# Performance work log

Hardware: AMD Instinct MI355X
Metric: run time of the kernel (lower is better)

Reference implementation:

```python
import jax, jax.numpy as jnp
import numpy as np

K, D, B = 2048, 50257, 256
N_CLASS = 2

def setup_inputs() -> dict:
    key = jax.random.key(0)
    k1, k2, k3 = jax.random.split(key, 3)
    # strictly positive (probability-like) entries so log() is finite
    queue_anchor = jax.random.uniform(k1, (K, D), dtype=jnp.float32, minval=1e-3, maxval=1.0)
    query = jax.random.uniform(k2, (B, D), dtype=jnp.float32, minval=1e-3, maxval=1.0)
    queue_label = jax.random.randint(k3, (K,), 0, N_CLASS, dtype=jnp.int64)
    return {"query": query, "queue_anchor": queue_anchor, "queue_label": queue_label}

def reference(query, queue_anchor, queue_label):
    # torch code: mean_d( a[:,None,:] * (log a[:,None,:] - log q) ).T  -> [B, K]
    # algebraically identical, avoiding the (K,B,D) intermediate:
    #   kl[b,k] = mean_d(a_k * log a_k) - (1/D) * sum_d a_k[d] * log q_b[d]
    d = queue_anchor.shape[1]
    self_term = jnp.mean(queue_anchor * jnp.log(queue_anchor), axis=1)        # [K]
    cross_term = jnp.einsum('kd,bd->kb', queue_anchor, jnp.log(query)) / d    # [K, B]
    kl_distance = (self_term[:, None] - cross_term).T                          # [B, K]
    # knn == 1 path: nearest anchor's label per query
    return queue_label[jnp.argmin(kl_distance, axis=1)]                        # [B]
```

## Files before the change

kernel.cpp:

```cpp
#include <hip/hip_runtime.h>


constexpr int K    = 2048;
constexpr int D    = 50257;
constexpr int B    = 256;
constexpr int DSPL = 25344;
constexpr int NC   = 8;
constexpr float MARGIN = 4.0f;

typedef __attribute__((ext_vector_type(8))) short bf16x8;
typedef __attribute__((ext_vector_type(4))) float f32x4;
typedef __attribute__((ext_vector_type(8))) unsigned short u16x8;

__device__ inline unsigned short f2bf_rne(float f) {
    union { float f; unsigned u; } v; v.f = f;
    unsigned r = v.u + 0x7FFFu + ((v.u >> 16) & 1u);
    return (unsigned short)(r >> 16);
}

__global__ __launch_bounds__(256)
void lq_kernel(const float* __restrict__ q, unsigned short* __restrict__ lq,
               int aoff, int DL, int nch)
{
    const int stride = gridDim.x * blockDim.x;
    const int total  = nch * B * 4;
    for (int c = blockIdx.x * blockDim.x + threadIdx.x; c < total; c += stride) {
        const int sub = c & 3;
        const int b   = (c >> 2) & 255;
        const int ch  = c >> 10;
        const int d0  = ch * 32 + sub * 8;
        u16x8 w;
#pragma unroll
        for (int j = 0; j < 8; ++j) {
            const int d = d0 + j;
            const float v = (d < DL) ? q[(size_t)b * D + aoff + d] : 1.f;
            w[j] = f2bf_rne(__logf(v));
        }
        *reinterpret_cast<u16x8*>(&lq[((size_t)ch * B + b) * 32 + sub * 8]) = w;
    }
}

__global__ __launch_bounds__(512)
void gemm_kernel(const float* __restrict__ anchor,
                 const unsigned short* __restrict__ lq,
                 float* __restrict__ part,
                 float* __restrict__ selfp,
                 int dc, int DL, int DCAP, int aoff, int zoff)
{
    const int nb8 = gridDim.x >> 3;
    const int g   = (blockIdx.x & 7) * nb8 + (blockIdx.x >> 3);
    const int z   = g >> 6;
    const int kt  = g & 63;
    const int k0  = kt * 32;

    const int t    = threadIdx.x;
    const int wid  = t >> 6;
    const int lane = t & 63;
    const int lr   = lane & 15;
    const int lg   = lane >> 4;

    const int zd0 = z * dc;
    const int zd1 = min(zd0 + dc, DCAP);
    const int wd  = ((dc / 8) + 31) & ~31;
    const int d0  = zd0 + wid * wd;
    const int d1  = min(d0 + wd, zd1);

    const size_t KDm4 = (size_t)K * D - 4;

    f32x4 acc0[16], acc1[16];
#pragma unroll
    for (int j = 0; j < 16; ++j)
#pragma unroll
        for (int i = 0; i < 4; ++i) { acc0[j][i] = 0.f; acc1[j][i] = 0.f; }

    float sacc0 = 0.f, sacc1 = 0.f;

    if (d0 < d1) {
        const int ar0 = k0 + lr;
        const int ar1 = ar0 + 16;
        const size_t gA0 = (size_t)ar0 * D + aoff + d0 + lg * 8;
        const size_t gA1 = (size_t)ar1 * D + aoff + d0 + lg * 8;
        const int ph0 = (int)(gA0 & 3);
        const int ph1 = (int)(gA1 & 3);
        size_t iA0 = gA0 - ph0;
        size_t iA1 = gA1 - ph1;

        const unsigned short* qp =
            lq + ((size_t)(d0 >> 5) * (B * 32) + (size_t)lr * 32 + lg * 8);

        auto ld4 = [&](size_t fi) -> float4 {
            if (fi > KDm4) fi = KDm4;
            return *reinterpret_cast<const float4*>(anchor + fi);
        };

        for (int dd = d0; dd < d1; dd += 32) {
            const int dbase = dd + lg * 8;
            bf16x8 af0, af1;
            {
                const float4 v0 = ld4(iA0), v1 = ld4(iA0 + 4), v2 = ld4(iA0 + 8);
                float wf[12] = {v0.x, v0.y, v0.z, v0.w, v1.x, v1.y, v1.z, v1.w,
                                v2.x, v2.y, v2.z, v2.w};
                float s9[9];
#pragma unroll
                for (int j = 0; j < 9; ++j) s9[j] = (ph0 & 2) ? wf[j + 2] : wf[j];
#pragma unroll
                for (int j = 0; j < 8; ++j) {
                    float a = (ph0 & 1) ? s9[j + 1] : s9[j];
                    a = (dbase + j < DL) ? a : 0.f;
                    if (a > 0.f) sacc0 = fmaf(a, __logf(a), sacc0);
                    af0[j] = (short)f2bf_rne(a);
                }
                iA0 += 32;
            }
            {
                const float4 v0 = ld4(iA1), v1 = ld4(iA1 + 4), v2 = ld4(iA1 + 8);
                float wf[12] = {v0.x, v0.y, v0.z, v0.w, v1.x, v1.y, v1.z, v1.w,
                                v2.x, v2.y, v2.z, v2.w};
                float s9[9];
#pragma unroll
                for (int j = 0; j < 9; ++j) s9[j] = (ph1 & 2) ? wf[j + 2] : wf[j];
#pragma unroll
                for (int j = 0; j < 8; ++j) {
                    float a = (ph1 & 1) ? s9[j + 1] : s9[j];
                    a = (dbase + j < DL) ? a : 0.f;
                    if (a > 0.f) sacc1 = fmaf(a, __logf(a), sacc1);
                    af1[j] = (short)f2bf_rne(a);
                }
                iA1 += 32;
            }
            {
                bf16x8 qf[8];
#pragma unroll
                for (int j = 0; j < 8; ++j)
                    qf[j] = *reinterpret_cast<const bf16x8*>(qp + j * 512);
#pragma unroll
                for (int j = 0; j < 8; ++j) {
                    acc0[j] = __builtin_amdgcn_mfma_f32_16x16x32_bf16(af0, qf[j], acc0[j], 0, 0, 0);
                    acc1[j] = __builtin_amdgcn_mfma_f32_16x16x32_bf16(af1, qf[j], acc1[j], 0, 0, 0);
                }
#pragma unroll
                for (int j = 0; j < 8; ++j)
                    qf[j] = *reinterpret_cast<const bf16x8*>(qp + (8 + j) * 512);
#pragma unroll
                for (int j = 0; j < 8; ++j) {
                    acc0[8 + j] = __builtin_amdgcn_mfma_f32_16x16x32_bf16(af0, qf[j], acc0[8 + j], 0, 0, 0);
                    acc1[8 + j] = __builtin_amdgcn_mfma_f32_16x16x32_bf16(af1, qf[j], acc1[8 + j], 0, 0, 0);
                }
            }
            qp += (size_t)B * 32;
        }
    }

    sacc0 += __shfl_xor(sacc0, 16); sacc0 += __shfl_xor(sacc0, 32);
    sacc1 += __shfl_xor(sacc1, 16); sacc1 += __shfl_xor(sacc1, 32);

    __shared__ __align__(16) float red[4][256 * 36];
    __shared__ float sred[8][32];

    if (lane < 16) { sred[wid][lr] = sacc0; sred[wid][16 + lr] = sacc1; }

    const int rbase = wid & 3;
    if (wid < 4) {
#pragma unroll
        for (int bt = 0; bt < 16; ++bt) {
            float* p0 = &red[rbase][(bt * 16 + lr) * 36 + lg * 4];
            *reinterpret_cast<f32x4*>(p0)      = acc0[bt];
            *reinterpret_cast<f32x4*>(p0 + 16) = acc1[bt];
        }
    }
    __syncthreads();
    if (wid >= 4) {
#pragma unroll
        for (int bt = 0; bt < 16; ++bt) {
            float* p0 = &red[rbase][(bt * 16 + lr) * 36 + lg * 4];
            f32x4 v0 = *reinterpret_cast<f32x4*>(p0);
            f32x4 v1 = *reinterpret_cast<f32x4*>(p0 + 16);
#pragma unroll
            for (int i = 0; i < 4; ++i) { v0[i] += acc0[bt][i]; v1[i] += acc1[bt][i]; }
            *reinterpret_cast<f32x4*>(p0)      = v0;
            *reinterpret_cast<f32x4*>(p0 + 16) = v1;
        }
    }
    __syncthreads();
    for (int i = t; i < 256 * 36; i += 512) {
        red[0][i] += red[2][i];
        red[1][i] += red[3][i];
    }
    __syncthreads();
    for (int i = t; i < 256 * 36; i += 512) red[0][i] += red[1][i];
    if (t < 32) {
        float s = 0.f;
#pragma unroll
        for (int w8 = 0; w8 < 8; ++w8) s += sred[w8][t];
        selfp[(size_t)(zoff + z) * K + k0 + t] = s;
    }
    __syncthreads();
    for (int i = t; i < 2048; i += 512) {
        const int b  = i >> 3;
        const int kq = i & 7;
        const f32x4 v = *reinterpret_cast<f32x4*>(&red[0][b * 36 + kq * 4]);
        *reinterpret_cast<f32x4*>(&part[((size_t)z * B + b) * K + k0 + kq * 4]) = v;
    }
}

__global__ __launch_bounds__(256)
void reduce_kernel(const float* __restrict__ part, float* __restrict__ crossA, int pch)
{
    const int i = blockIdx.x * 256 + threadIdx.x;
    const f32x4* p4 = reinterpret_cast<const f32x4*>(part);
    f32x4 s = p4[i];
    for (int z = 1; z < pch; ++z) {
        const f32x4 v = p4[(size_t)z * (B * K / 4) + i];
#pragma unroll
        for (int j = 0; j < 4; ++j) s[j] += v[j];
    }
    reinterpret_cast<f32x4*>(crossA)[i] = s;
}

__global__ __launch_bounds__(256)
void selfsum_kernel(const float* __restrict__ selfp, float* __restrict__ selftot, int rows)
{
    const int k = blockIdx.x * 256 + threadIdx.x;
    float s = 0.f;
    for (int z = 0; z < rows; ++z) s += selfp[(size_t)z * K + k];
    selftot[k] = s;
}

__global__ __launch_bounds__(256)
void topk_kernel(const float* __restrict__ crossA, const float* __restrict__ part,
                 const float* __restrict__ selftot,
                 int* __restrict__ cand, int* __restrict__ need, int pch)
{
    const int b = blockIdx.x, t = threadIdx.x;
    float v[8];
#pragma unroll
    for (int i = 0; i < 8; ++i) {
        const int k = i * 256 + t;
        float cv = crossA[(size_t)b * K + k];
        for (int z = 0; z < pch; ++z) cv += part[((size_t)z * B + b) * K + k];
        v[i] = selftot[k] - cv;
    }
    __shared__ float sv[256];
    __shared__ int   si[256];
    __shared__ float topv[2];
    for (int r = 0; r < NC; ++r) {
        float bv = 3.4e38f; int bk = K;
#pragma unroll
        for (int i = 0; i < 8; ++i) {
            const int k = i * 256 + t;
            if (v[i] < bv) { bv = v[i]; bk = k; }
        }
        sv[t] = bv; si[t] = bk;
        __syncthreads();
        for (int off = 128; off > 0; off >>= 1) {
            if (t < off) {
                if (sv[t + off] < sv[t] || (sv[t + off] == sv[t] && si[t + off] < si[t])) {
                    sv[t] = sv[t + off]; si[t] = si[t + off];
                }
            }
            __syncthreads();
        }
        const int kwin = si[0];
        if ((kwin & 255) == t) v[kwin >> 8] = 3.4e38f;
        if (t == 0) {
            cand[b * NC + r] = kwin;
            if (r < 2) topv[r] = sv[0];
        }
        __syncthreads();
    }
    if (t == 0) need[b] = (topv[1] - topv[0] < MARGIN) ? 1 : 0;
}

__global__ __launch_bounds__(512)
void rescore_kernel(const float* __restrict__ query, const float* __restrict__ anchor,
                    const int* __restrict__ cand, const int* __restrict__ need,
                    double* __restrict__ pp)
{
    const int b = blockIdx.x, h = blockIdx.y, t = threadIdx.x;
    if (!need[b]) return;
    const int dlo = h * 25129;
    const int dhi = min(D, dlo + 25129);
    int ks[NC];
#pragma unroll
    for (int c = 0; c < NC; ++c) ks[c] = cand[b * NC + c];
    const float* qrow = query + (size_t)b * D;

    double a8[NC];
#pragma unroll
    for (int c = 0; c < NC; ++c) a8[c] = 0.0;

    for (int d = dlo + t; d < dhi; d += 512) {
        const double lqv = (double)logf(qrow[d]);
#pragma unroll
        for (int c = 0; c < NC; ++c)
            a8[c] = fma((double)anchor[(size_t)ks[c] * D + d], lqv, a8[c]);
    }

    __shared__ double red[512];
    for (int c = 0; c < NC; ++c) {
        red[t] = a8[c];
        __syncthreads();
        for (int off = 256; off > 0; off >>= 1) {
            if (t < off) red[t] += red[t + off];
            __syncthreads();
        }
        if (t == 0) pp[((size_t)b * 2 + h) * NC + c] = red[0];
        __syncthreads();
    }
}

__global__ __launch_bounds__(256)
void final_kernel(const double* __restrict__ pp, const float* __restrict__ selftot,
                  const int* __restrict__ cand, const int* __restrict__ need,
                  const int* __restrict__ label, int* __restrict__ out)
{
    const int b = threadIdx.x;
    if (!need[b]) { out[b] = label[cand[b * NC]]; return; }
    float best = 3.4e38f; int bk = K;
#pragma unroll
    for (int c = 0; c < NC; ++c) {
        const int k = cand[b * NC + c];
        const double cv = pp[((size_t)b * 2 + 0) * NC + c] + pp[((size_t)b * 2 + 1) * NC + c];
        const float sc = selftot[k] - (float)cv;
        if (sc < best || (sc == best && k < bk)) { best = sc; bk = k; }
    }
    out[b] = label[bk];
}

extern "C" void kernel_launch(void* const* d_in, const int* in_sizes, int n_in,
                              void* d_out, int out_size, void* d_ws, size_t ws_size,
                              hipStream_t stream)
{
    const float* query  = (const float*)d_in[0];
    const float* anchor = (const float*)d_in[1];
    const int*   label  = (const int*)d_in[2];
    int* out = (int*)d_out;

    const int DL1 = DSPL;
    const int DL2 = D - DSPL;
    const int nch1 = (DL1 + 31) / 32;
    const int nch2 = (DL2 + 31) / 32;
    const int nchmax = nch1;

    size_t cur = 0;
    auto alloc = [&](size_t bytes) -> void* {
        cur = (cur + 255) & ~(size_t)255;
        void* p = (char*)d_ws + cur;
        cur += bytes;
        return p;
    };

    unsigned short* lq      = (unsigned short*)alloc((size_t)nchmax * B * 32 * 2);
    float*          crossA  = (float*)alloc((size_t)B * K * 4);
    float*          selfp   = (float*)alloc((size_t)12 * K * 4);
    float*          selftot = (float*)alloc((size_t)K * 4);
    int*            cand    = (int*)alloc((size_t)B * NC * 4);
    int*            need    = (int*)alloc((size_t)B * 4);
    double*         pp      = (double*)alloc((size_t)B * 2 * NC * 8);
    const size_t fixed_end  = cur;

    int pch = 1;
    for (int s = 4; s >= 1; s >>= 1) {
        if (fixed_end + (size_t)s * B * K * 4 + 256 <= ws_size) { pch = s; break; }
    }
    float* part = (float*)alloc((size_t)pch * B * K * 4);

    const int dc1 = ((DL1 + pch - 1) / pch + 31) & ~31;
    const int dc2 = ((DL2 + pch - 1) / pch + 31) & ~31;

    lq_kernel<<<2048, 256, 0, stream>>>(query, lq, 0, DL1, nch1);
    gemm_kernel<<<64 * pch, 512, 0, stream>>>(anchor, lq, part, selfp,
                                              dc1, DL1, nch1 * 32, 0, 0);
    reduce_kernel<<<B * K / 4 / 256, 256, 0, stream>>>(part, crossA, pch);

    lq_kernel<<<2048, 256, 0, stream>>>(query, lq, DSPL, DL2, nch2);
    gemm_kernel<<<64 * pch, 512, 0, stream>>>(anchor, lq, part, selfp,
                                              dc2, DL2, nch2 * 32, DSPL, pch);

    selfsum_kernel<<<K / 256, 256, 0, stream>>>(selfp, selftot, 2 * pch);
    topk_kernel<<<B, 256, 0, stream>>>(crossA, part, selftot, cand, need, pch);
    rescore_kernel<<<dim3(B, 2), 512, 0, stream>>>(query, anchor, cand, need, pp);
    final_kernel<<<1, 256, 0, stream>>>(pp, selftot, cand, need, label, out);
}
```

Before: 536.9 us.

## Halve K-tile per GEMM block to 16 rows and double grid size

Each GEMM block now handles 16 anchor rows instead of 32, so the launch grid doubles and per-thread accumulator registers halve, which can raise occupancy and spread work across more CUs. The LDS reduction buffer shrinks to match. A fast path also skips per-element bounds checks and the positivity test on interior chunks. The trade-off is that query bf16 fragments are now reloaded per 16 rows, which doubles query traffic relative to MFMA work.

```diff
diff --git a/kernel.cpp b/kernel.cpp
--- a/kernel.cpp
+++ b/kernel.cpp
@@ -49,9 +49,9 @@
 {
     const int nb8 = gridDim.x >> 3;
     const int g   = (blockIdx.x & 7) * nb8 + (blockIdx.x >> 3);
-    const int z   = g >> 6;
-    const int kt  = g & 63;
-    const int k0  = kt * 32;
+    const int z   = g >> 7;
+    const int kt  = g & 127;
+    const int k0  = kt * 16;
 
     const int t    = threadIdx.x;
     const int wid  = t >> 6;
@@ -67,23 +67,19 @@
 
     const size_t KDm4 = (size_t)K * D - 4;
 
-    f32x4 acc0[16], acc1[16];
+    f32x4 acc[16];
 #pragma unroll
     for (int j = 0; j < 16; ++j)
 #pragma unroll
-        for (int i = 0; i < 4; ++i) { acc0[j][i] = 0.f; acc1[j][i] = 0.f; }
-
-    float sacc0 = 0.f, sacc1 = 0.f;
+        for (int i = 0; i < 4; ++i) acc[j][i] = 0.f;
+
+    float sacc = 0.f;
 
     if (d0 < d1) {
-        const int ar0 = k0 + lr;
-        const int ar1 = ar0 + 16;
-        const size_t gA0 = (size_t)ar0 * D + aoff + d0 + lg * 8;
-        const size_t gA1 = (size_t)ar1 * D + aoff + d0 + lg * 8;
-        const int ph0 = (int)(gA0 & 3);
-        const int ph1 = (int)(gA1 & 3);
-        size_t iA0 = gA0 - ph0;
-        size_t iA1 = gA1 - ph1;
+        const int ar = k0 + lr;
+        const size_t gA = (size_t)ar * D + aoff + d0 + lg * 8;
+        const int ph = (int)(gA & 3);
+        size_t iA = gA - ph;
 
         const unsigned short* qp =
             lq + ((size_t)(d0 >> 5) * (B * 32) + (size_t)lr * 32 + lg * 8);
@@ -94,111 +90,91 @@
         };
 
         for (int dd = d0; dd < d1; dd += 32) {
-            const int dbase = dd + lg * 8;
-            bf16x8 af0, af1;
+            bf16x8 af;
             {
-                const float4 v0 = ld4(iA0), v1 = ld4(iA0 + 4), v2 = ld4(iA0 + 8);
+                const float4 v0 = ld4(iA), v1 = ld4(iA + 4), v2 = ld4(iA + 8);
                 float wf[12] = {v0.x, v0.y, v0.z, v0.w, v1.x, v1.y, v1.z, v1.w,
                                 v2.x, v2.y, v2.z, v2.w};
                 float s9[9];
 #pragma unroll
-                for (int j = 0; j < 9; ++j) s9[j] = (ph0 & 2) ? wf[j + 2] : wf[j];
-#pragma unroll
-                for (int j = 0; j < 8; ++j) {
-                    float a = (ph0 & 1) ? s9[j + 1] : s9[j];
-                    a = (dbase + j < DL) ? a : 0.f;
-                    if (a > 0.f) sacc0 = fmaf(a, __logf(a), sacc0);
-                    af0[j] = (short)f2bf_rne(a);
+                for (int j = 0; j < 9; ++j) s9[j] = (ph & 2) ? wf[j + 2] : wf[j];
+                if (dd + 32 <= DL) {
+#pragma unroll
+                    for (int j = 0; j < 8; ++j) {
+                        const float a = (ph & 1) ? s9[j + 1] : s9[j];
+                        sacc = fmaf(a, __logf(a), sacc);
+                        af[j] = (short)f2bf_rne(a);
+                    }
+                } else {
+                    const int dbase = dd + lg * 8;
+#pragma unroll
+                    for (int j = 0; j < 8; ++j) {
+                        float a = (ph & 1) ? s9[j + 1] : s9[j];
+                        a = (dbase + j < DL) ? a : 0.f;
+                        if (a > 0.f) sacc = fmaf(a, __logf(a), sacc);
+                        af[j] = (short)f2bf_rne(a);
+                    }
                 }
-                iA0 += 32;
+                iA += 32;
             }
-            {
-                const float4 v0 = ld4(iA1), v1 = ld4(iA1 + 4), v2 = ld4(iA1 + 8);
-                float wf[12] = {v0.x, v0.y, v0.z, v0.w, v1.x, v1.y, v1.z, v1.w,
-                                v2.x, v2.y, v2.z, v2.w};
-                float s9[9];
-#pragma unroll
-                for (int j = 0; j < 9; ++j) s9[j] = (ph1 & 2) ? wf[j + 2] : wf[j];
-#pragma unroll
-                for (int j = 0; j < 8; ++j) {
-                    float a = (ph1 & 1) ? s9[j + 1] : s9[j];
-                    a = (dbase + j < DL) ? a : 0.f;
-                    if (a > 0.f) sacc1 = fmaf(a, __logf(a), sacc1);
-                    af1[j] = (short)f2bf_rne(a);
-                }
-                iA1 += 32;
-            }
-            {
-                bf16x8 qf[8];
-#pragma unroll
-                for (int j = 0; j < 8; ++j)
-                    qf[j] = *reinterpret_cast<const bf16x8*>(qp + j * 512);
-#pragma unroll
-                for (int j = 0; j < 8; ++j) {
-                    acc0[j] = __builtin_amdgcn_mfma_f32_16x16x32_bf16(af0, qf[j], acc0[j], 0, 0, 0);
-                    acc1[j] = __builtin_amdgcn_mfma_f32_16x16x32_bf16(af1, qf[j], acc1[j], 0, 0, 0);
-                }
-#pragma unroll
-                for (int j = 0; j < 8; ++j)
-                    qf[j] = *reinterpret_cast<const bf16x8*>(qp + (8 + j) * 512);
-#pragma unroll
-                for (int j = 0; j < 8; ++j) {
-                    acc0[8 + j] = __builtin_amdgcn_mfma_f32_16x16x32_bf16(af0, qf[j], acc0[8 + j], 0, 0, 0);
-                    acc1[8 + j] = __builtin_amdgcn_mfma_f32_16x16x32_bf16(af1, qf[j], acc1[8 + j], 0, 0, 0);
-                }
+#pragma unroll
+            for (int h = 0; h < 4; ++h) {
+                bf16x8 qf[4];
+#pragma unroll
+                for (int j = 0; j < 4; ++j)
+                    qf[j] = *reinterpret_cast<const bf16x8*>(qp + (h * 4 + j) * 512);
+#pragma unroll
+                for (int j = 0; j < 4; ++j)
+                    acc[h * 4 + j] = __builtin_amdgcn_mfma_f32_16x16x32_bf16(
+                        af, qf[j], acc[h * 4 + j], 0, 0, 0);
             }
             qp += (size_t)B * 32;
         }
     }
 
-    sacc0 += __shfl_xor(sacc0, 16); sacc0 += __shfl_xor(sacc0, 32);
-    sacc1 += __shfl_xor(sacc1, 16); sacc1 += __shfl_xor(sacc1, 32);
-
-    __shared__ __align__(16) float red[4][256 * 36];
-    __shared__ float sred[8][32];
-
-    if (lane < 16) { sred[wid][lr] = sacc0; sred[wid][16 + lr] = sacc1; }
-
-    const int rbase = wid & 3;
+    sacc += __shfl_xor(sacc, 16);
+    sacc += __shfl_xor(sacc, 32);
+
+    __shared__ __align__(16) float red[4][256 * 18];
+    __shared__ float sred[8][16];
+
+    if (lane < 16) sred[wid][lr] = sacc;
+
+    const int rb = wid & 3;
     if (wid < 4) {
 #pragma unroll
-        for (int bt = 0; bt < 16; ++bt) {
-            float* p0 = &red[rbase][(bt * 16 + lr) * 36 + lg * 4];
-            *reinterpret_cast<f32x4*>(p0)      = acc0[bt];
-            *reinterpret_cast<f32x4*>(p0 + 16) = acc1[bt];
-        }
+        for (int bt = 0; bt < 16; ++bt)
+            *reinterpret_cast<f32x4*>(&red[rb][(bt * 16 + lr) * 18 + lg * 4]) = acc[bt];
     }
     __syncthreads();
     if (wid >= 4) {
 #pragma unroll
         for (int bt = 0; bt < 16; ++bt) {
-            float* p0 = &red[rbase][(bt * 16 + lr) * 36 + lg * 4];
-            f32x4 v0 = *reinterpret_cast<f32x4*>(p0);
-            f32x4 v1 = *reinterpret_cast<f32x4*>(p0 + 16);
-#pragma unroll
-            for (int i = 0; i < 4; ++i) { v0[i] += acc0[bt][i]; v1[i] += acc1[bt][i]; }
-            *reinterpret_cast<f32x4*>(p0)      = v0;
-            *reinterpret_cast<f32x4*>(p0 + 16) = v1;
+            float* p0 = &red[rb][(bt * 16 + lr) * 18 + lg * 4];
+            f32x4 v = *reinterpret_cast<f32x4*>(p0);
+#pragma unroll
+            for (int i = 0; i < 4; ++i) v[i] += acc[bt][i];
+            *reinterpret_cast<f32x4*>(p0) = v;
         }
     }
     __syncthreads();
-    for (int i = t; i < 256 * 36; i += 512) {
+    for (int i = t; i < 256 * 18; i += 512) {
         red[0][i] += red[2][i];
         red[1][i] += red[3][i];
     }
     __syncthreads();
-    for (int i = t; i < 256 * 36; i += 512) red[0][i] += red[1][i];
-    if (t < 32) {
+    for (int i = t; i < 256 * 18; i += 512) red[0][i] += red[1][i];
+    if (t < 16) {
         float s = 0.f;
 #pragma unroll
         for (int w8 = 0; w8 < 8; ++w8) s += sred[w8][t];
         selfp[(size_t)(zoff + z) * K + k0 + t] = s;
     }
     __syncthreads();
-    for (int i = t; i < 2048; i += 512) {
-        const int b  = i >> 3;
-        const int kq = i & 7;
-        const f32x4 v = *reinterpret_cast<f32x4*>(&red[0][b * 36 + kq * 4]);
+    for (int i = t; i < 1024; i += 512) {
+        const int b  = i >> 2;
+        const int kq = i & 3;
+        const f32x4 v = *reinterpret_cast<f32x4*>(&red[0][b * 18 + kq * 4]);
         *reinterpret_cast<f32x4*>(&part[((size_t)z * B + b) * K + k0 + kq * 4]) = v;
     }
 }
@@ -369,13 +345,13 @@
     const int dc2 = ((DL2 + pch - 1) / pch + 31) & ~31;
 
     lq_kernel<<<2048, 256, 0, stream>>>(query, lq, 0, DL1, nch1);
-    gemm_kernel<<<64 * pch, 512, 0, stream>>>(anchor, lq, part, selfp,
-                                              dc1, DL1, nch1 * 32, 0, 0);
+    gemm_kernel<<<128 * pch, 512, 0, stream>>>(anchor, lq, part, selfp,
+                                               dc1, DL1, nch1 * 32, 0, 0);
     reduce_kernel<<<B * K / 4 / 256, 256, 0, stream>>>(part, crossA, pch);
 
     lq_kernel<<<2048, 256, 0, stream>>>(query, lq, DSPL, DL2, nch2);
-    gemm_kernel<<<64 * pch, 512, 0, stream>>>(anchor, lq, part, selfp,
-                                              dc2, DL2, nch2 * 32, DSPL, pch);
+    gemm_kernel<<<128 * pch, 512, 0, stream>>>(anchor, lq, part, selfp,
+                                               dc2, DL2, nch2 * 32, DSPL, pch);
 
     selfsum_kernel<<<K / 256, 256, 0, stream>>>(selfp, selftot, 2 * pch);
     topk_kernel<<<B, 256, 0, stream>>>(crossA, part, selftot, cand, need, pch);
```

Result: slower. 698.5 us (+30.1%).
